# Optimization experiments

Measured on AMD Instinct MI355X. Metric: run time of the kernel, lower is better.

Reference implementation:

```python
import jax, jax.numpy as jnp
import numpy as np

N, E, F_IN, EDIM, HEADS, DIM = 100000, 1600000, 128, 16, 4, 16
HC = HEADS * DIM


def add_self_loops_mean(src, dst, ea, n):
    # PyG add_self_loops with fill_value='mean': self-loop edge_attr is the mean
    # of incoming-edge attrs per target node (0 for isolated nodes).
    cnt = jax.ops.segment_sum(jnp.ones((dst.shape[0],), ea.dtype), dst, num_segments=n)
    sm = jax.ops.segment_sum(ea, dst, num_segments=n)
    loop = jnp.where(cnt[:, None] > 0, sm / jnp.maximum(cnt, 1.0)[:, None], 0.0)
    idx = jnp.arange(n, dtype=src.dtype)
    return (jnp.concatenate([src, idx]), jnp.concatenate([dst, idx]),
            jnp.concatenate([ea, loop], axis=0))


def gatv2(x, src, dst, ea, Wl, bl, Wr, br, We, att, bias):
    n = x.shape[0]
    h, c = att.shape
    xl = (x @ Wl + bl).reshape(n, h, c)   # source transform (lin_l)
    xr = (x @ Wr + br).reshape(n, h, c)   # target transform (lin_r)
    ee = (ea @ We).reshape(-1, h, c)      # edge transform (lin_edge, no bias)
    s = jax.nn.leaky_relu(xl[src] + xr[dst] + ee, negative_slope=0.2)  # [E,h,c]
    alpha = jnp.einsum('ehc,hc->eh', s, att)                           # [E,h]
    amax = jax.ops.segment_max(alpha, dst, num_segments=n)
    amax = jnp.where(jnp.isfinite(amax), amax, 0.0)
    ex = jnp.exp(alpha - amax[dst])
    denom = jax.ops.segment_sum(ex, dst, num_segments=n)
    a = ex / (denom[dst] + 1e-16)                                      # segment softmax
    out = jax.ops.segment_sum(xl[src] * a[:, :, None], dst, num_segments=n)
    return out.reshape(n, h * c) + bias


def setup_inputs() -> dict:
    key = jax.random.key(0)
    ks = jax.random.split(key, 24)
    s = 0.1
    d = {
        'x': jax.random.normal(ks[0], (N, F_IN), jnp.float32),
        'edge_index': jax.random.randint(ks[1], (2, E), 0, N, jnp.int32),
        'edge_attr': jax.random.normal(ks[2], (E, EDIM), jnp.float32),
        'Wl1': jax.random.normal(ks[3], (F_IN, HC)) * s, 'bl1': jnp.zeros((HC,)),
        'Wr1': jax.random.normal(ks[4], (F_IN, HC)) * s, 'br1': jnp.zeros((HC,)),
        'We1': jax.random.normal(ks[5], (EDIM, HC)) * s,
        'att1': jax.random.normal(ks[6], (HEADS, DIM)) * s,
        'bias1': jnp.zeros((HC,)),
        'Wl2': jax.random.normal(ks[7], (HC, HC)) * s, 'bl2': jnp.zeros((HC,)),
        'Wr2': jax.random.normal(ks[8], (HC, HC)) * s, 'br2': jnp.zeros((HC,)),
        'We2': jax.random.normal(ks[9], (EDIM, HC)) * s,
        'att2': jax.random.normal(ks[10], (HEADS, DIM)) * s,
        'bias2': jnp.zeros((HC,)),
        'W_lin1': jax.random.normal(ks[11], (HC, DIM)) * s, 'b_lin1': jnp.zeros((DIM,)),
        'W_lin2': jax.random.normal(ks[12], (DIM, 1)) * s, 'b_lin2': jnp.zeros((1,)),
    }
    return d


def reference(x, edge_index, edge_attr, Wl1, bl1, Wr1, br1, We1, att1, bias1,
              Wl2, bl2, Wr2, br2, We2, att2, bias2,
              W_lin1, b_lin1, W_lin2, b_lin2):
    src, dst, ea = add_self_loops_mean(edge_index[0], edge_index[1], edge_attr, x.shape[0])
    h = jax.nn.relu(gatv2(x, src, dst, ea, Wl1, bl1, Wr1, br1, We1, att1, bias1))
    h = jax.nn.relu(gatv2(h, src, dst, ea, Wl2, bl2, Wr2, br2, We2, att2, bias2))
    h = jax.nn.relu(h @ W_lin1 + b_lin1)
    # dropout p=0.1 is identity in eval mode
    out = jax.nn.sigmoid((h @ W_lin2 + b_lin2)[:, 0])
    return out
```

## Files before the change

### kernel.cpp

```cpp
#include <hip/hip_runtime.h>
#include <stdint.h>

typedef unsigned short u16;
typedef unsigned int u32;
typedef unsigned long long u64;

typedef __attribute__((ext_vector_type(8))) short bfrag;
typedef __attribute__((ext_vector_type(4))) float f32x4;

__device__ __forceinline__ float bf2f(u16 u) { return __uint_as_float(((u32)u) << 16); }
__device__ __forceinline__ u16 f2bf(float f) {
    u32 i = __float_as_uint(f);
    u32 r = i + 0x7fffu + ((i >> 16) & 1u);
    return (u16)(r >> 16);
}
__device__ __forceinline__ float lo16(u32 u) { return __uint_as_float(u << 16); }
__device__ __forceinline__ float hi16(u32 u) { return __uint_as_float(u & 0xffff0000u); }
__device__ __forceinline__ u32 pack2(float a, float b) {
    return (u32)f2bf(a) | ((u32)f2bf(b) << 16);
}
#define RFL(x) __builtin_amdgcn_readfirstlane(x)

#define DPP_ROR_ADD(p, ctrl) \
    p += __int_as_float(__builtin_amdgcn_update_dpp(0, __float_as_int(p), ctrl, 0xF, 0xF, false))
__device__ __forceinline__ float red16(float p) {
    DPP_ROR_ADD(p, 0x128);
    DPP_ROR_ADD(p, 0x124);
    DPP_ROR_ADD(p, 0x122);
    DPP_ROR_ADD(p, 0x121);
    return p;
}

__global__ void deg_hist(const int* __restrict__ dst, int E, int* __restrict__ deg) {
    int e = blockIdx.x * blockDim.x + threadIdx.x;
    if (e < E) atomicAdd(&deg[dst[e]], 1);
}

#define SCAN_T 256
#define SCAN_E 8
#define SCAN_CHUNK 2048

__global__ void scan_partial(const int* __restrict__ deg, int n, int* __restrict__ partials) {
    __shared__ int sh[SCAN_T];
    int b = blockIdx.x, t = threadIdx.x;
    int base = b * SCAN_CHUNK + t * SCAN_E;
    int s = 0;
#pragma unroll
    for (int i = 0; i < SCAN_E; i++) { int idx = base + i; if (idx < n) s += deg[idx]; }
    sh[t] = s; __syncthreads();
    for (int off = SCAN_T / 2; off > 0; off >>= 1) {
        if (t < off) sh[t] += sh[t + off];
        __syncthreads();
    }
    if (t == 0) partials[b] = sh[0];
}

__global__ void scan_mid(int* __restrict__ partials, int nb) {
    if (threadIdx.x == 0 && blockIdx.x == 0) {
        int acc = 0;
        for (int i = 0; i < nb; i++) { int v = partials[i]; partials[i] = acc; acc += v; }
    }
}

__global__ void scan_final(const int* __restrict__ deg, int n, const int* __restrict__ partials,
                           int* __restrict__ offs, int E) {
    __shared__ int sh[SCAN_T];
    int b = blockIdx.x, t = threadIdx.x;
    int base = b * SCAN_CHUNK + t * SCAN_E;
    int loc[SCAN_E];
    int s = 0;
#pragma unroll
    for (int i = 0; i < SCAN_E; i++) {
        int idx = base + i;
        int v = (idx < n) ? deg[idx] : 0;
        loc[i] = s; s += v;
    }
    sh[t] = s; __syncthreads();
    for (int off = 1; off < SCAN_T; off <<= 1) {
        int v = 0;
        if (t >= off) v = sh[t - off];
        __syncthreads();
        if (t >= off) sh[t] += v;
        __syncthreads();
    }
    int tbase = partials[b] + sh[t] - s;
#pragma unroll
    for (int i = 0; i < SCAN_E; i++) { int idx = base + i; if (idx < n) offs[idx] = tbase + loc[i]; }
    if (b == gridDim.x - 1 && t == SCAN_T - 1) offs[n] = E;
}

template <int RS>
__global__ void csr_fill_ea(const int* __restrict__ srcv, const int* __restrict__ dstv,
                            const float4* __restrict__ ea, int E,
                            int* __restrict__ cursor, u32* __restrict__ rec) {
    int e = blockIdx.x * blockDim.x + threadIdx.x;
    if (e >= E) return;
    const float4* s = ea + (u64)e * 4;
    float4 v0 = s[0], v1 = s[1], v2 = s[2], v3 = s[3];
    u32 a0 = pack2(v0.x, v0.y), a1 = pack2(v0.z, v0.w);
    u32 a2 = pack2(v1.x, v1.y), a3 = pack2(v1.z, v1.w);
    u32 a4 = pack2(v2.x, v2.y), a5 = pack2(v2.z, v2.w);
    u32 a6 = pack2(v3.x, v3.y), a7 = pack2(v3.z, v3.w);
    int sr = srcv[e];
    int d = dstv[e];
    int p = atomicAdd(&cursor[d], 1);
    u32* r = rec + (u64)p * RS;
    if (RS == 16) {
        uint4* q = (uint4*)r;
        q[0] = make_uint4((u32)sr, 0u, a0, a1);
        q[1] = make_uint4(a2, a3, a4, a5);
        q[2] = make_uint4(a6, a7, 0u, 0u);
        q[3] = make_uint4(0u, 0u, 0u, 0u);
    } else {
        u64* q = (u64*)r;
        q[0] = (u64)(u32)sr;
        q[1] = (u64)a0 | ((u64)a1 << 32);
        q[2] = (u64)a2 | ((u64)a3 << 32);
        q[3] = (u64)a4 | ((u64)a5 << 32);
        q[4] = (u64)a6 | ((u64)a7 << 32);
    }
}

template <int RS>
__global__ void loop_mean(const int* __restrict__ offs, const u16* __restrict__ rec16, int N,
                          u16* __restrict__ loop_ea) {
    int t = blockIdx.x * blockDim.x + threadIdx.x;
    if (t < N * 16) {
        int n = t >> 4, k = t & 15;
        int a = offs[n], b = offs[n + 1];
        float s0 = 0.f, s1 = 0.f, s2 = 0.f, s3 = 0.f;
        int p = a;
        for (; p + 4 <= b; p += 4) {
            s0 += bf2f(rec16[(u64)p * (2 * RS) + 4 + k]);
            s1 += bf2f(rec16[(u64)(p + 1) * (2 * RS) + 4 + k]);
            s2 += bf2f(rec16[(u64)(p + 2) * (2 * RS) + 4 + k]);
            s3 += bf2f(rec16[(u64)(p + 3) * (2 * RS) + 4 + k]);
        }
        for (; p < b; p++) s0 += bf2f(rec16[(u64)p * (2 * RS) + 4 + k]);
        float s = (s0 + s1) + (s2 + s3);
        float m = (b > a) ? s / (float)(b - a) : 0.f;
        loop_ea[t] = f2bf(m);
    }
}

template <int K>
__global__ void pack_w(const float* __restrict__ Wl, const float* __restrict__ Wr,
                       u32* __restrict__ Wb) {
    constexpr int NKS = K / 32;
    int t = blockIdx.x * blockDim.x + threadIdx.x;
    if (t >= 8 * NKS * 64) return;
    int lane = t & 63;
    int ks = (t >> 6) % NKS;
    int ct = (t >> 6) / NKS;
    int n = lane & 15, quad = lane >> 4;
    int c = ct * 16 + n;
    const float* W = (c < 64) ? Wl : Wr;
    int cc = c & 63;
    u32* d = Wb + (u64)t * 4;
#pragma unroll
    for (int p = 0; p < 4; p++) {
        int k0 = ks * 32 + quad * 8 + 2 * p;
        d[p] = pack2(W[(u64)k0 * 64 + cc], W[(u64)(k0 + 1) * 64 + cc]);
    }
}

template <int K, bool XF32>
__global__ __launch_bounds__(256) void gemm_mfma(const void* __restrict__ Xv,
                                                 const u32* __restrict__ Wb,
                                                 const float* __restrict__ bl,
                                                 const float* __restrict__ br,
                                                 int N, u16* __restrict__ xl, u16* __restrict__ xr) {
    constexpr int NKS = K / 32;
    int lane = threadIdx.x & 63;
    int gw = (blockIdx.x * 256 + threadIdx.x) >> 6;
    int row0 = gw * 16;
    if (row0 >= N) return;
    int m = lane & 15, quad = lane >> 4;

    f32x4 acc[8];
#pragma unroll
    for (int ct = 0; ct < 8; ct++) acc[ct] = (f32x4){0.f, 0.f, 0.f, 0.f};

#pragma unroll
    for (int ks = 0; ks < NKS; ks++) {
        bfrag a;
        if (XF32) {
            const float* xp = (const float*)Xv + (u64)(row0 + m) * K + ks * 32 + quad * 8;
            float4 v0 = *(const float4*)xp;
            float4 v1 = *(const float4*)(xp + 4);
            union { bfrag v; u32 d[4]; } au;
            au.d[0] = pack2(v0.x, v0.y); au.d[1] = pack2(v0.z, v0.w);
            au.d[2] = pack2(v1.x, v1.y); au.d[3] = pack2(v1.z, v1.w);
            a = au.v;
        } else {
            a = *(const bfrag*)((const u16*)Xv + (u64)(row0 + m) * K + ks * 32 + quad * 8);
        }
#pragma unroll
        for (int ct = 0; ct < 8; ct++) {
            bfrag b = *(const bfrag*)(Wb + (u64)((ct * NKS + ks) * 64 + lane) * 4);
            acc[ct] = __builtin_amdgcn_mfma_f32_16x16x32_bf16(a, b, acc[ct], 0, 0, 0);
        }
    }

#pragma unroll
    for (int ct = 0; ct < 8; ct++) {
        float bv = (ct < 4) ? bl[ct * 16 + m] : br[(ct - 4) * 16 + m];
        u16* dbuf = (ct < 4) ? xl : xr;
        int cc = (ct & 3) * 16 + m;
#pragma unroll
        for (int r = 0; r < 4; r++) {
            int row = row0 + quad * 4 + r;
            dbuf[(u64)row * 64 + cc] = f2bf(acc[ct][r] + bv);
        }
    }
}

template <int RS>
__global__ __launch_bounds__(256) void gat_layer(const u16* __restrict__ xl, const u16* __restrict__ xr,
                                                 const int* __restrict__ offs, const u32* __restrict__ rec,
                                                 const u16* __restrict__ loop_ea,
                                                 const float* __restrict__ We,
                                                 const float* __restrict__ att,
                                                 const float* __restrict__ bias,
                                                 int N, u16* __restrict__ out) {
    int l = threadIdx.x & 63;
    int wid = RFL((int)((blockIdx.x * 256 + threadIdx.x) >> 6));
    int nw = gridDim.x * 4;
    float wec[16];
#pragma unroll
    for (int k = 0; k < 16; k++) wec[k] = We[k * 64 + l];
    float att_l = att[l];
    float bias_l = bias[l];
    const u32* le = (const u32*)loop_ea;

    for (int n = wid; n < N; n += nw) {
        float xr_l = bf2f(xr[(u32)(n * 64 + l)]);
        int a = RFL(offs[n]);
        int b = RFL(offs[n + 1]);
        float lsum = 0.f, o = 0.f;

        auto edge_u = [&](const u32* eap, int srcn) {
            float xlv = bf2f(xl[(u32)(srcn * 64 + l)]);
            float z = xr_l;
#pragma unroll
            for (int k = 0; k < 8; k++) {
                u32 u = eap[k];
                z = fmaf(lo16(u), wec[2 * k], z);
                z = fmaf(hi16(u), wec[2 * k + 1], z);
            }
            z += xlv;
            z = fmaxf(z, 0.2f * z);
            float w = __expf(red16(z * att_l));
            lsum += w;
            o = fmaf(w, xlv, o);
        };

        edge_u(le + (u64)n * 8, n);
        int i = a;
        for (; i < b - 1; i += 2) {
            const u32* e0 = rec + (u64)i * RS;
            const u32* e1 = rec + (u64)(i + 1) * RS;
            int s0 = RFL((int)e0[0]);
            int s1 = RFL((int)e1[0]);
            edge_u(e0 + 2, s0);
            edge_u(e1 + 2, s1);
        }
        if (i < b) {
            const u32* e0 = rec + (u64)i * RS;
            edge_u(e0 + 2, RFL((int)e0[0]));
        }

        float res = o / (lsum + 1e-16f) + bias_l;
        res = fmaxf(res, 0.f);
        out[(u32)(n * 64 + l)] = f2bf(res);
    }
}

__global__ __launch_bounds__(256) void mlp_head(const u16* __restrict__ h,
                                                const float* __restrict__ W1, const float* __restrict__ b1,
                                                const float* __restrict__ W2, const float* __restrict__ b2,
                                                int N, float* __restrict__ out) {
    __shared__ float w1[64 * 16];
    __shared__ float sb1[16];
    __shared__ float w2[16];
    for (int i = threadIdx.x; i < 64 * 16; i += 256) w1[i] = W1[i];
    if (threadIdx.x < 16) { sb1[threadIdx.x] = b1[threadIdx.x]; w2[threadIdx.x] = W2[threadIdx.x]; }
    __syncthreads();
    float b2v = b2[0];
    int n = blockIdx.x * blockDim.x + threadIdx.x;
    if (n < N) {
        float hv[64];
        const u32* hp = (const u32*)(h + (u64)n * 64);
#pragma unroll
        for (int i = 0; i < 32; i++) { u32 u = hp[i]; hv[2 * i] = lo16(u); hv[2 * i + 1] = hi16(u); }
        float z = b2v;
        for (int j = 0; j < 16; j++) {
            float acc = sb1[j];
#pragma unroll
            for (int k = 0; k < 64; k++) acc = fmaf(hv[k], w1[k * 16 + j], acc);
            acc = fmaxf(acc, 0.f);
            z = fmaf(acc, w2[j], z);
        }
        out[n] = 1.f / (1.f + __expf(-z));
    }
}

struct Args {
    const float *x, *ea;
    const int *srcv, *dstv;
    const float *Wl1, *bl1, *Wr1, *br1, *We1, *att1, *bias1;
    const float *Wl2, *bl2, *Wr2, *br2, *We2, *att2, *bias2;
    const float *W1, *b1, *W2, *b2;
    float* out;
    int N, E;
    int *deg, *cursor, *offs, *partials;
    u32 *rec, *wb1, *wb2;
    u16 *loop_ea, *xl, *xr, *hb;
};

template <int RS>
static void run_pipeline(const Args& A, hipStream_t stream) {
    const int B = 256;
    int N = A.N, E = A.E;

    hipMemsetAsync(A.deg, 0, (size_t)N * 4, stream);
    pack_w<128><<<8, 256, 0, stream>>>(A.Wl1, A.Wr1, A.wb1);
    pack_w<64><<<4, 256, 0, stream>>>(A.Wl2, A.Wr2, A.wb2);

    deg_hist<<<(E + B - 1) / B, B, 0, stream>>>(A.dstv, E, A.deg);
    int nb = (N + SCAN_CHUNK - 1) / SCAN_CHUNK;
    scan_partial<<<nb, SCAN_T, 0, stream>>>(A.deg, N, A.partials);
    scan_mid<<<1, 64, 0, stream>>>(A.partials, nb);
    scan_final<<<nb, SCAN_T, 0, stream>>>(A.deg, N, A.partials, A.offs, E);
    hipMemcpyAsync(A.cursor, A.offs, (size_t)N * 4, hipMemcpyDeviceToDevice, stream);
    csr_fill_ea<RS><<<(E + B - 1) / B, B, 0, stream>>>(A.srcv, A.dstv, (const float4*)A.ea, E,
                                                       A.cursor, A.rec);
    loop_mean<RS><<<(16 * N + B - 1) / B, B, 0, stream>>>(A.offs, (const u16*)A.rec, N, A.loop_ea);

    int gemm_blocks = (N / 16 + 3) / 4;
    gemm_mfma<128, true><<<gemm_blocks, 256, 0, stream>>>(A.x, A.wb1, A.bl1, A.br1, N, A.xl, A.xr);
    gat_layer<RS><<<8192, 256, 0, stream>>>(A.xl, A.xr, A.offs, A.rec, A.loop_ea,
                                            A.We1, A.att1, A.bias1, N, A.hb);
    gemm_mfma<64, false><<<gemm_blocks, 256, 0, stream>>>(A.hb, A.wb2, A.bl2, A.br2, N, A.xl, A.xr);
    gat_layer<RS><<<8192, 256, 0, stream>>>(A.xl, A.xr, A.offs, A.rec, A.loop_ea,
                                            A.We2, A.att2, A.bias2, N, A.hb);
    mlp_head<<<(N + B - 1) / B, B, 0, stream>>>(A.hb, A.W1, A.b1, A.W2, A.b2, N, A.out);
}

extern "C" void kernel_launch(void* const* d_in, const int* in_sizes, int n_in,
                              void* d_out, int out_size, void* d_ws, size_t ws_size,
                              hipStream_t stream) {
    Args A;
    A.x    = (const float*)d_in[0];
    const int* ei = (const int*)d_in[1];
    A.ea   = (const float*)d_in[2];
    A.Wl1  = (const float*)d_in[3];  A.bl1 = (const float*)d_in[4];
    A.Wr1  = (const float*)d_in[5];  A.br1 = (const float*)d_in[6];
    A.We1  = (const float*)d_in[7];  A.att1 = (const float*)d_in[8];  A.bias1 = (const float*)d_in[9];
    A.Wl2  = (const float*)d_in[10]; A.bl2 = (const float*)d_in[11];
    A.Wr2  = (const float*)d_in[12]; A.br2 = (const float*)d_in[13];
    A.We2  = (const float*)d_in[14]; A.att2 = (const float*)d_in[15]; A.bias2 = (const float*)d_in[16];
    A.W1   = (const float*)d_in[17]; A.b1 = (const float*)d_in[18];
    A.W2   = (const float*)d_in[19]; A.b2 = (const float*)d_in[20];
    A.out  = (float*)d_out;

    A.N = in_sizes[0] / 128;
    A.E = in_sizes[1] / 2;
    A.srcv = ei;
    A.dstv = ei + A.E;
    const int N = A.N, E = A.E;

    size_t need16 = (size_t)E * 64 + (size_t)N * (4 + 4 + 4 + 32 + 128 + 128 + 128) + (1u << 21);
    int RS = (ws_size >= need16) ? 16 : 10;

    uint8_t* p = (uint8_t*)d_ws;
    auto carve = [&](size_t bytes) -> void* {
        void* r = (void*)p;
        p += (bytes + 255) & ~(size_t)255;
        return r;
    };
    A.deg     = (int*)carve((size_t)N * 4);
    A.cursor  = (int*)carve((size_t)N * 4);
    A.offs    = (int*)carve((size_t)(N + 1) * 4);
    A.partials= (int*)carve(4096);
    A.rec     = (u32*)carve((size_t)E * 4 * RS);
    A.loop_ea = (u16*)carve((size_t)N * 16 * 2);
    A.xl      = (u16*)carve((size_t)N * 64 * 2);
    A.xr      = (u16*)carve((size_t)N * 64 * 2);
    A.hb      = (u16*)carve((size_t)N * 64 * 2);
    A.wb1     = (u32*)carve(8 * 4 * 64 * 16);
    A.wb2     = (u32*)carve(8 * 2 * 64 * 16);
    (void)ws_size; (void)n_in; (void)out_size;

    if (RS == 16) run_pipeline<16>(A, stream);
    else          run_pipeline<10>(A, stream);
}
```

Before: 648.9 us.

## Fold self-loop mean edge attr into GAT layer via linearity; use bf16 dot2

Removes the loop_mean kernel and its buffer. Because the edge transform is linear, the self-loop edge embedding equals the mean of the per-edge projected embeddings, so gat_layer accumulates those projections and handles the self-loop after the neighbour loop. The edge-attr projection also switches to the bf16 fdot2 builtin when available, with the weights packed to bf16. This changes numerics slightly (weights rounded to bf16, and the self-loop is now processed last) and trades one extra pass over the records for a few extra ALU ops per edge.

```diff
diff --git a/kernel.cpp b/kernel.cpp
--- a/kernel.cpp
+++ b/kernel.cpp
@@ -7,6 +7,13 @@
 
 typedef __attribute__((ext_vector_type(8))) short bfrag;
 typedef __attribute__((ext_vector_type(4))) float f32x4;
+
+#if __has_builtin(__builtin_amdgcn_fdot2_f32_bf16)
+#define HAS_DOT2 1
+typedef __attribute__((ext_vector_type(2))) __bf16 bf16x2;
+#else
+#define HAS_DOT2 0
+#endif
 
 __device__ __forceinline__ float bf2f(u16 u) { return __uint_as_float(((u32)u) << 16); }
 __device__ __forceinline__ u16 f2bf(float f) {
@@ -121,28 +128,6 @@
     }
 }
 
-template <int RS>
-__global__ void loop_mean(const int* __restrict__ offs, const u16* __restrict__ rec16, int N,
-                          u16* __restrict__ loop_ea) {
-    int t = blockIdx.x * blockDim.x + threadIdx.x;
-    if (t < N * 16) {
-        int n = t >> 4, k = t & 15;
-        int a = offs[n], b = offs[n + 1];
-        float s0 = 0.f, s1 = 0.f, s2 = 0.f, s3 = 0.f;
-        int p = a;
-        for (; p + 4 <= b; p += 4) {
-            s0 += bf2f(rec16[(u64)p * (2 * RS) + 4 + k]);
-            s1 += bf2f(rec16[(u64)(p + 1) * (2 * RS) + 4 + k]);
-            s2 += bf2f(rec16[(u64)(p + 2) * (2 * RS) + 4 + k]);
-            s3 += bf2f(rec16[(u64)(p + 3) * (2 * RS) + 4 + k]);
-        }
-        for (; p < b; p++) s0 += bf2f(rec16[(u64)p * (2 * RS) + 4 + k]);
-        float s = (s0 + s1) + (s2 + s3);
-        float m = (b > a) ? s / (float)(b - a) : 0.f;
-        loop_ea[t] = f2bf(m);
-    }
-}
-
 template <int K>
 __global__ void pack_w(const float* __restrict__ Wl, const float* __restrict__ Wr,
                        u32* __restrict__ Wb) {
@@ -218,7 +203,6 @@
 template <int RS>
 __global__ __launch_bounds__(256) void gat_layer(const u16* __restrict__ xl, const u16* __restrict__ xr,
                                                  const int* __restrict__ offs, const u32* __restrict__ rec,
-                                                 const u16* __restrict__ loop_ea,
                                                  const float* __restrict__ We,
                                                  const float* __restrict__ att,
                                                  const float* __restrict__ bias,
@@ -226,36 +210,55 @@
     int l = threadIdx.x & 63;
     int wid = RFL((int)((blockIdx.x * 256 + threadIdx.x) >> 6));
     int nw = gridDim.x * 4;
+#if HAS_DOT2
+    bf16x2 wec[8];
+#pragma unroll
+    for (int k = 0; k < 8; k++) {
+        union { u32 u; bf16x2 v; } wu;
+        wu.u = pack2(We[(2 * k) * 64 + l], We[(2 * k + 1) * 64 + l]);
+        wec[k] = wu.v;
+    }
+#else
     float wec[16];
 #pragma unroll
     for (int k = 0; k < 16; k++) wec[k] = We[k * 64 + l];
+#endif
     float att_l = att[l];
     float bias_l = bias[l];
-    const u32* le = (const u32*)loop_ea;
 
     for (int n = wid; n < N; n += nw) {
         float xr_l = bf2f(xr[(u32)(n * 64 + l)]);
+        float xl_self = bf2f(xl[(u32)(n * 64 + l)]);
         int a = RFL(offs[n]);
         int b = RFL(offs[n + 1]);
-        float lsum = 0.f, o = 0.f;
+        float lsum = 0.f, o = 0.f, eesum = 0.f;
 
         auto edge_u = [&](const u32* eap, int srcn) {
             float xlv = bf2f(xl[(u32)(srcn * 64 + l)]);
-            float z = xr_l;
+            float ee = 0.f;
+#if HAS_DOT2
+#pragma unroll
+            for (int k = 0; k < 8; k++) {
+                union { u32 u; bf16x2 v; } au;
+                au.u = eap[k];
+                ee = __builtin_amdgcn_fdot2_f32_bf16(au.v, wec[k], ee, false);
+            }
+#else
 #pragma unroll
             for (int k = 0; k < 8; k++) {
                 u32 u = eap[k];
-                z = fmaf(lo16(u), wec[2 * k], z);
-                z = fmaf(hi16(u), wec[2 * k + 1], z);
+                ee = fmaf(lo16(u), wec[2 * k], ee);
+                ee = fmaf(hi16(u), wec[2 * k + 1], ee);
             }
-            z += xlv;
+#endif
+            eesum += ee;
+            float z = (ee + xr_l) + xlv;
             z = fmaxf(z, 0.2f * z);
             float w = __expf(red16(z * att_l));
             lsum += w;
             o = fmaf(w, xlv, o);
         };
 
-        edge_u(le + (u64)n * 8, n);
         int i = a;
         for (; i < b - 1; i += 2) {
             const u32* e0 = rec + (u64)i * RS;
@@ -268,6 +271,16 @@
         if (i < b) {
             const u32* e0 = rec + (u64)i * RS;
             edge_u(e0 + 2, RFL((int)e0[0]));
+        }
+
+        {
+            int deg = b - a;
+            float inv = (deg > 0) ? 1.f / (float)deg : 0.f;
+            float z = (eesum * inv + xr_l) + xl_self;
+            z = fmaxf(z, 0.2f * z);
+            float w = __expf(red16(z * att_l));
+            lsum += w;
+            o = fmaf(w, xl_self, o);
         }
 
         float res = o / (lsum + 1e-16f) + bias_l;
@@ -315,7 +328,7 @@
     int N, E;
     int *deg, *cursor, *offs, *partials;
     u32 *rec, *wb1, *wb2;
-    u16 *loop_ea, *xl, *xr, *hb;
+    u16 *xl, *xr, *hb;
 };
 
 template <int RS>
@@ -335,14 +348,13 @@
     hipMemcpyAsync(A.cursor, A.offs, (size_t)N * 4, hipMemcpyDeviceToDevice, stream);
     csr_fill_ea<RS><<<(E + B - 1) / B, B, 0, stream>>>(A.srcv, A.dstv, (const float4*)A.ea, E,
                                                        A.cursor, A.rec);
-    loop_mean<RS><<<(16 * N + B - 1) / B, B, 0, stream>>>(A.offs, (const u16*)A.rec, N, A.loop_ea);
 
     int gemm_blocks = (N / 16 + 3) / 4;
     gemm_mfma<128, true><<<gemm_blocks, 256, 0, stream>>>(A.x, A.wb1, A.bl1, A.br1, N, A.xl, A.xr);
-    gat_layer<RS><<<8192, 256, 0, stream>>>(A.xl, A.xr, A.offs, A.rec, A.loop_ea,
+    gat_layer<RS><<<8192, 256, 0, stream>>>(A.xl, A.xr, A.offs, A.rec,
                                             A.We1, A.att1, A.bias1, N, A.hb);
     gemm_mfma<64, false><<<gemm_blocks, 256, 0, stream>>>(A.hb, A.wb2, A.bl2, A.br2, N, A.xl, A.xr);
-    gat_layer<RS><<<8192, 256, 0, stream>>>(A.xl, A.xr, A.offs, A.rec, A.loop_ea,
+    gat_layer<RS><<<8192, 256, 0, stream>>>(A.xl, A.xr, A.offs, A.rec,
                                             A.We2, A.att2, A.bias2, N, A.hb);
     mlp_head<<<(N + B - 1) / B, B, 0, stream>>>(A.hb, A.W1, A.b1, A.W2, A.b2, N, A.out);
 }
@@ -370,7 +382,7 @@
     A.dstv = ei + A.E;
     const int N = A.N, E = A.E;
 
-    size_t need16 = (size_t)E * 64 + (size_t)N * (4 + 4 + 4 + 32 + 128 + 128 + 128) + (1u << 21);
+    size_t need16 = (size_t)E * 64 + (size_t)N * (4 + 4 + 4 + 128 + 128 + 128) + (1u << 21);
     int RS = (ws_size >= need16) ? 16 : 10;
 
     uint8_t* p = (uint8_t*)d_ws;
@@ -384,7 +396,6 @@
     A.offs    = (int*)carve((size_t)(N + 1) * 4);
     A.partials= (int*)carve(4096);
     A.rec     = (u32*)carve((size_t)E * 4 * RS);
-    A.loop_ea = (u16*)carve((size_t)N * 16 * 2);
     A.xl      = (u16*)carve((size_t)N * 64 * 2);
     A.xr      = (u16*)carve((size_t)N * 64 * 2);
     A.hb      = (u16*)carve((size_t)N * 64 * 2);
```

Result: no change. 637.8 us (-1.7%).
